# Optimization experiments

Measured on AMD Instinct MI355X. Metric: run time of the kernel, lower is better.

## Reference

```python
import jax, jax.numpy as jnp
import numpy as np

VOCAB, EMB, HID, LAYERS, SEQ, BATCH = 10000, 1024, 1024, 2, 64, 64


def setup_inputs() -> dict:
    key = jax.random.key(0)
    ks = jax.random.split(key, 12)
    b = 1.0 / np.sqrt(HID)
    u = lambda k, shape, bd: jax.random.uniform(k, shape, jnp.float32, -bd, bd)
    return {
        "inputs": jax.random.randint(ks[0], (SEQ, BATCH), 0, VOCAB),
        "hidden": jnp.zeros((LAYERS, BATCH, HID), jnp.float32),
        "emb": u(ks[1], (VOCAB, EMB), 0.1),
        "W0": u(ks[2], (EMB, 3 * HID), b),
        "U0": u(ks[3], (HID, 3 * HID), b),
        "bw0": u(ks[4], (3 * HID,), b),
        "bu0": u(ks[5], (3 * HID,), b),
        "W1": u(ks[6], (HID, 3 * HID), b),
        "U1": u(ks[7], (HID, 3 * HID), b),
        "bw1": u(ks[8], (3 * HID,), b),
        "bu1": u(ks[9], (3 * HID,), b),
        "fcW": u(ks[10], (VOCAB, HID), 0.1),
        "fcb": jnp.zeros((VOCAB,), jnp.float32),
    }


def gru_cell(x, h, W, U, bw, bu):
    gx = x @ W + bw            # [B, 3H]
    gh = h @ U + bu            # [B, 3H]
    i_r, i_z, i_n = jnp.split(gx, 3, axis=1)
    h_r, h_z, h_n = jnp.split(gh, 3, axis=1)
    r = jax.nn.sigmoid(i_r + h_r)
    z = jax.nn.sigmoid(i_z + h_z)
    h_tilde = jnp.tanh(i_n + r * h_n)
    return (1.0 - z) * h + z * h_tilde


def reference(inputs, hidden, emb, W0, U0, bw0, bu0, W1, U1, bw1, bu1, fcW, fcb):
    # dp_keep_prob = 1.0 -> dropout is identity (eval-mode reference)
    def step(hid, tok):
        x = emb[tok]                                   # [B, EMB]
        h0 = gru_cell(x, hid[0], W0, U0, bw0, bu0)     # [B, H]
        h1 = gru_cell(h0, hid[1], W1, U1, bw1, bu1)    # [B, H]
        y = h1 @ fcW.T + fcb                           # [B, V]
        return jnp.stack([h0, h1]), y

    hidden_f, logits = jax.lax.scan(step, hidden, inputs)
    return logits, hidden_f
```

## Files before the change

kernel.cpp:

```cpp
#include <hip/hip_runtime.h>
#include <math.h>

#define SEQL 64
#define BATCHN 64
#define HID 1024
#define EMBD 1024
#define VOCAB 10000
#define G3 3072
#define NPAD 10240
#define AROWS 4096
#define HSLOT 65536

typedef float f4v __attribute__((ext_vector_type(4)));
typedef unsigned short us4 __attribute__((ext_vector_type(4)));
typedef unsigned short us8 __attribute__((ext_vector_type(8)));
typedef __bf16 bf8v __attribute__((ext_vector_type(8)));

__device__ __forceinline__ unsigned short f2bf(float f) {
    unsigned u = __float_as_uint(f);
    u += 0x7fffu + ((u >> 16) & 1u);
    return (unsigned short)(u >> 16);
}
__device__ __forceinline__ float bf2f(unsigned short h) {
    return __uint_as_float(((unsigned)h) << 16);
}
__device__ __forceinline__ void split2(float f, unsigned short &hi, unsigned short &lo) {
    hi = f2bf(f);
    lo = f2bf(f - bf2f(hi));
}
__device__ __forceinline__ f4v mfma16(us8 a, us8 b, f4v c) {
    return __builtin_amdgcn_mfma_f32_16x16x32_bf16(
        __builtin_bit_cast(bf8v, a), __builtin_bit_cast(bf8v, b), c, 0, 0, 0);
}
__device__ __forceinline__ float sigmoidf_(float x) { return 1.f / (1.f + expf(-x)); }

__device__ __forceinline__ size_t htile_off(int b, int j) {
    return ((size_t)((((b >> 4) * 32 + (j >> 5)) * 64) + ((j >> 3) & 3) * 16 + (b & 15))) * 8 + (j & 7);
}

__global__ __launch_bounds__(256)
void tile_weights_kernel(const float* __restrict__ U0, const float* __restrict__ W1,
                         const float* __restrict__ U1, const float* __restrict__ W0,
                         unsigned short* __restrict__ hi, unsigned short* __restrict__ lo)
{
    __shared__ float tile[32][65];
    const int mat = blockIdx.z;
    const float* src = (mat == 0) ? U0 : (mat == 1) ? W1 : (mat == 2) ? U1 : W0;
    const int n0 = blockIdx.x * 64, k0 = blockIdx.y * 32;
    const int t = threadIdx.x, tx = t & 63, ty = t >> 6;
#pragma unroll
    for (int s = 0; s < 8; s++)
        tile[ty * 8 + s][tx] = src[(size_t)(k0 + ty * 8 + s) * G3 + n0 + tx];
    __syncthreads();
    const int c = t >> 6, lane = t & 63, fr = lane & 15, kg = lane >> 4;
    const int cc = (n0 >> 4) + c;
    const size_t off = (((size_t)(mat * 192 + cc) * 32 + (k0 >> 5)) * 64 + lane) * 8;
    us8 h8, l8;
#pragma unroll
    for (int e = 0; e < 8; e++) {
        unsigned short a, b;
        split2(tile[kg * 8 + e][c * 16 + fr], a, b);
        h8[e] = a; l8[e] = b;
    }
    *(us8*)(hi + off) = h8;
    *(us8*)(lo + off) = l8;
}

__global__ void fc_pad_split_kernel(const float* __restrict__ fcW,
                                    unsigned short* __restrict__ hi, unsigned short* __restrict__ lo)
{
    size_t i = ((size_t)blockIdx.x * 256 + threadIdx.x) * 4;
    size_t row = i >> 10;
    f4v v = {0.f, 0.f, 0.f, 0.f};
    if (row < VOCAB) v = *(const f4v*)(fcW + i);
    us4 h, l;
#pragma unroll
    for (int j = 0; j < 4; j++) { unsigned short a, b; split2(v[j], a, b); h[j] = a; l[j] = b; }
    *(us4*)(hi + i) = h;
    *(us4*)(lo + i) = l;
}

__global__ void fcb_pad_kernel(const float* __restrict__ fcb, float* __restrict__ fcb_pad)
{
    int idx = blockIdx.x * 256 + threadIdx.x;
    if (idx < NPAD) fcb_pad[idx] = (idx < VOCAB) ? fcb[idx] : 0.f;
}

__global__ void small_prep_kernel(const float* __restrict__ hidden,
                                  unsigned short* __restrict__ h0th, unsigned short* __restrict__ h0tl,
                                  unsigned short* __restrict__ h1th, unsigned short* __restrict__ h1tl)
{
    int idx = blockIdx.x * 256 + threadIdx.x;
    if (idx < BATCHN * HID) {
        int b = idx >> 10, j = idx & 1023;
        size_t o = htile_off(b, j);
        unsigned short a1, b1;
        split2(hidden[idx], a1, b1);                 h0th[o] = a1; h0tl[o] = b1;
        split2(hidden[BATCHN * HID + idx], a1, b1);  h1th[o] = a1; h1tl[o] = b1;
    }
}

__global__ __launch_bounds__(256)
void gx0_gemm_kernel(const int* __restrict__ tok, const float* __restrict__ emb,
                     const unsigned short* __restrict__ Wthi, const unsigned short* __restrict__ Wtlo,
                     float* __restrict__ C)
{
    __shared__ unsigned short Ah[128][40], Al[128][40];
    const int bswz = blockIdx.x;
    const int xcd = bswz & 7, s = bswz >> 3;
    const int col0 = (xcd + 8 * (s >> 5)) * 128;
    const int row0 = (s & 31) * 128;
    const int tid = threadIdx.x;
    const int lane = tid & 63, wave = tid >> 6;
    const int wm = wave >> 1, wn = wave & 1;
    const int srow = tid >> 1;
    const int shalf = (tid & 1) * 16;

    const float* asrc = emb + (size_t)tok[row0 + srow] * EMBD + shalf;
    const int fr = lane & 15, fk = (lane >> 4) * 8;
    const int cc0 = (col0 >> 4) + wn * 4;

    f4v a[4];
#pragma unroll
    for (int q = 0; q < 4; q++) a[q] = *(const f4v*)(asrc + q * 4);

    f4v acc[4][4] = {};
    for (int k0 = 0; k0 < EMBD; k0 += 32) {
        __syncthreads();
        us8 ahv[2], alv[2];
#pragma unroll
        for (int q = 0; q < 4; q++)
#pragma unroll
            for (int j = 0; j < 4; j++) {
                unsigned short h, l;
                split2(a[q][j], h, l);
                ahv[q >> 1][(q & 1) * 4 + j] = h;
                alv[q >> 1][(q & 1) * 4 + j] = l;
            }
        *(us8*)(&Ah[srow][shalf]) = ahv[0];     *(us8*)(&Ah[srow][shalf + 8]) = ahv[1];
        *(us8*)(&Al[srow][shalf]) = alv[0];     *(us8*)(&Al[srow][shalf + 8]) = alv[1];
        __syncthreads();
        if (k0 + 32 < EMBD) {
#pragma unroll
            for (int q = 0; q < 4; q++) a[q] = *(const f4v*)(asrc + k0 + 32 + q * 4);
        }
        const int ks = k0 >> 5;
        us8 bfh[4], bfl[4];
#pragma unroll
        for (int n = 0; n < 4; n++) {
            const size_t bo = (((size_t)(3 * 192 + cc0 + n) * 32 + ks) * 64 + lane) * 8;
            bfh[n] = *(const us8*)(Wthi + bo);
            bfl[n] = *(const us8*)(Wtlo + bo);
        }
        us8 afh[4], afl[4];
#pragma unroll
        for (int m = 0; m < 4; m++) {
            afh[m] = *(const us8*)(&Ah[wm * 64 + m * 16 + fr][fk]);
            afl[m] = *(const us8*)(&Al[wm * 64 + m * 16 + fr][fk]);
        }
#pragma unroll
        for (int n = 0; n < 4; n++)
#pragma unroll
            for (int m = 0; m < 4; m++) {
                acc[m][n] = mfma16(afh[m], bfh[n], acc[m][n]);
                acc[m][n] = mfma16(afh[m], bfl[n], acc[m][n]);
                acc[m][n] = mfma16(afl[m], bfh[n], acc[m][n]);
            }
    }
    const int fq = lane >> 4;
#pragma unroll
    for (int m = 0; m < 4; m++)
#pragma unroll
        for (int n = 0; n < 4; n++)
#pragma unroll
            for (int i = 0; i < 4; i++) {
                int r = row0 + wm * 64 + m * 16 + fq * 4 + i;
                int c = col0 + wn * 64 + n * 16 + fr;
                C[(size_t)r * G3 + c] = acc[m][n][i];
            }
}

__global__ __launch_bounds__(256)
void logits_gemm_kernel(const unsigned short* __restrict__ h1t_hi, const unsigned short* __restrict__ h1t_lo,
                        const unsigned short* __restrict__ Bhi, const unsigned short* __restrict__ Blo,
                        const float* __restrict__ bias, float* __restrict__ C)
{
    __shared__ unsigned short Bh[128][40], Bl[128][40];
    const int bswz = blockIdx.x;
    const int xcd = bswz & 7, s = bswz >> 3;
    const int col0 = (xcd + 8 * (s >> 5)) * 128;
    const int row0 = (s & 31) * 128;
    const int t0 = row0 >> 6;
    const int tid = threadIdx.x;
    const int lane = tid & 63, wave = tid >> 6;
    const int wm = wave >> 1, wn = wave & 1;
    const int srow = tid >> 1;
    const int shalf = (tid & 1) * 16;

    const unsigned short* bh_src = Bhi + (size_t)(col0 + srow) * HID + shalf;
    const unsigned short* bl_src = Blo + (size_t)(col0 + srow) * HID + shalf;

    f4v acc[4][4] = {};
    us8 bh2[2], bl2[2];
    bh2[0] = *(const us8*)(bh_src);  bh2[1] = *(const us8*)(bh_src + 8);
    bl2[0] = *(const us8*)(bl_src);  bl2[1] = *(const us8*)(bl_src + 8);

    const int fr = lane & 15, fk = (lane >> 4) * 8;
    const size_t abase = ((size_t)(t0 + wm) * 128) * 512 + (size_t)lane * 8;

    for (int k0 = 0; k0 < HID; k0 += 32) {
        __syncthreads();
        *(us8*)(&Bh[srow][shalf]) = bh2[0];  *(us8*)(&Bh[srow][shalf + 8]) = bh2[1];
        *(us8*)(&Bl[srow][shalf]) = bl2[0];  *(us8*)(&Bl[srow][shalf + 8]) = bl2[1];
        __syncthreads();
        if (k0 + 32 < HID) {
            bh2[0] = *(const us8*)(bh_src + k0 + 32);  bh2[1] = *(const us8*)(bh_src + k0 + 40);
            bl2[0] = *(const us8*)(bl_src + k0 + 32);  bl2[1] = *(const us8*)(bl_src + k0 + 40);
        }
        const int ks = k0 >> 5;
        us8 afh[4], afl[4];
#pragma unroll
        for (int m = 0; m < 4; m++) {
            const size_t ao = abase + (size_t)(m * 32 + ks) * 512;
            afh[m] = *(const us8*)(h1t_hi + ao);
            afl[m] = *(const us8*)(h1t_lo + ao);
        }
#pragma unroll
        for (int n = 0; n < 4; n++) {
            us8 bfh = *(const us8*)(&Bh[wn * 64 + n * 16 + fr][fk]);
            us8 bfl = *(const us8*)(&Bl[wn * 64 + n * 16 + fr][fk]);
#pragma unroll
            for (int m = 0; m < 4; m++) {
                acc[m][n] = mfma16(afh[m], bfh, acc[m][n]);
                acc[m][n] = mfma16(afh[m], bfl, acc[m][n]);
                acc[m][n] = mfma16(afl[m], bfh, acc[m][n]);
            }
        }
    }
    const int fq = lane >> 4;
#pragma unroll
    for (int m = 0; m < 4; m++)
#pragma unroll
        for (int n = 0; n < 4; n++)
#pragma unroll
            for (int i = 0; i < 4; i++) {
                int r = row0 + wm * 64 + m * 16 + fq * 4 + i;
                int c = col0 + wn * 64 + n * 16 + fr;
                float v = acc[m][n][i] + bias[c];
                if (c < VOCAB) C[(size_t)r * VOCAB + c] = v;
            }
}

template <bool DO_L0, bool DO_L1>
__global__ __launch_bounds__(512)
void step_kernel(const unsigned short* __restrict__ h0hi, const unsigned short* __restrict__ h0lo,
                 const unsigned short* __restrict__ h1hi, const unsigned short* __restrict__ h1lo,
                 const unsigned short* __restrict__ Wthi, const unsigned short* __restrict__ Wtlo,
                 const float* __restrict__ gx0next,
                 const float* __restrict__ bw0, const float* __restrict__ bu0,
                 const float* __restrict__ bw1, const float* __restrict__ bu1,
                 unsigned short* __restrict__ h0o_hi, unsigned short* __restrict__ h0o_lo,
                 unsigned short* __restrict__ h1o_hi, unsigned short* __restrict__ h1o_lo)
{
    __shared__ float red[4][9][16][17];
    const int tid = threadIdx.x, lane = tid & 63, wave = tid >> 6;
    const int bswz = blockIdx.x;
    const int xcd = bswz & 7, sb = bswz >> 3;
    const int jc = xcd + 8 * (sb >> 2);
    const int wr = sb & 3;
    const int j0 = jc * 16;
    const int T0 = DO_L0 ? 0 : 3, T1 = DO_L1 ? 9 : 3;

    f4v acc[9] = {};
#pragma unroll 2
    for (int ksl = 0; ksl < 4; ksl++) {
        const int ks = wave * 4 + ksl;
        const size_t aoff = ((size_t)(wr * 32 + ks) * 64 + lane) * 8;
        us8 a0h = *(const us8*)(h0hi + aoff);
        us8 a0l = *(const us8*)(h0lo + aoff);
        us8 a1h = {}, a1l = {};
        if (DO_L1) { a1h = *(const us8*)(h1hi + aoff); a1l = *(const us8*)(h1lo + aoff); }
#pragma unroll
        for (int g = 0; g < 3; g++) {
            const size_t base = (((size_t)(g * 64 + jc) * 32 + ks) * 64 + lane) * 8;
            if (DO_L0) {
                us8 bh = *(const us8*)(Wthi + base);
                us8 bl = *(const us8*)(Wtlo + base);
                acc[g] = mfma16(a0h, bh, acc[g]);
                acc[g] = mfma16(a0h, bl, acc[g]);
                acc[g] = mfma16(a0l, bh, acc[g]);
            }
            if (DO_L1) {
                const size_t b1 = base + (size_t)192 * 32 * 64 * 8;
                us8 bh = *(const us8*)(Wthi + b1);
                us8 bl = *(const us8*)(Wtlo + b1);
                acc[3 + g] = mfma16(a0h, bh, acc[3 + g]);
                acc[3 + g] = mfma16(a0h, bl, acc[3 + g]);
                acc[3 + g] = mfma16(a0l, bh, acc[3 + g]);
                const size_t b2 = base + (size_t)2 * 192 * 32 * 64 * 8;
                us8 ch = *(const us8*)(Wthi + b2);
                us8 cl = *(const us8*)(Wtlo + b2);
                acc[6 + g] = mfma16(a1h, ch, acc[6 + g]);
                acc[6 + g] = mfma16(a1h, cl, acc[6 + g]);
                acc[6 + g] = mfma16(a1l, ch, acc[6 + g]);
            }
        }
    }
    const int rrow = (lane >> 4) * 4, rcol = lane & 15;
    if (wave >= 4) {
#pragma unroll
        for (int t2 = 0; t2 < 9; t2++) if (t2 >= T0 && t2 < T1)
#pragma unroll
            for (int i = 0; i < 4; i++) red[wave - 4][t2][rrow + i][rcol] = acc[t2][i];
    }
    __syncthreads();
    if (wave < 4) {
#pragma unroll
        for (int t2 = 0; t2 < 9; t2++) if (t2 >= T0 && t2 < T1)
#pragma unroll
            for (int i = 0; i < 4; i++)
                red[wave][t2][rrow + i][rcol] += acc[t2][i];
    }
    __syncthreads();
    if (tid < 256) {
        const int bl_ = tid >> 4, jl = tid & 15;
        const int b = wr * 16 + bl_, j = j0 + jl;
        float G[9];
#pragma unroll
        for (int t2 = 0; t2 < 9; t2++) if (t2 >= T0 && t2 < T1)
            G[t2] = (red[0][t2][bl_][jl] + red[1][t2][bl_][jl])
                  + (red[2][t2][bl_][jl] + red[3][t2][bl_][jl]);
        const size_t po = htile_off(b, j);
        if (DO_L0) {
            float sr = gx0next[(size_t)b * G3 + j]            + bw0[j]           + G[0] + bu0[j];
            float sz = gx0next[(size_t)b * G3 + HID + j]      + bw0[HID + j]     + G[1] + bu0[HID + j];
            float gxn = gx0next[(size_t)b * G3 + 2 * HID + j] + bw0[2 * HID + j];
            float ghn = G[2] + bu0[2 * HID + j];
            float r = sigmoidf_(sr);
            float z = sigmoidf_(sz);
            float ht = tanhf(gxn + r * ghn);
            float hp = bf2f(h0hi[po]) + bf2f(h0lo[po]);
            float hn = (1.f - z) * hp + z * ht;
            unsigned short hh, hl2; split2(hn, hh, hl2);
            h0o_hi[po] = hh; h0o_lo[po] = hl2;
        }
        if (DO_L1) {
            float sr = G[3] + bw1[j]           + G[6] + bu1[j];
            float sz = G[4] + bw1[HID + j]     + G[7] + bu1[HID + j];
            float gxn = G[5] + bw1[2 * HID + j];
            float ghn = G[8] + bu1[2 * HID + j];
            float r = sigmoidf_(sr);
            float z = sigmoidf_(sz);
            float ht = tanhf(gxn + r * ghn);
            float hp = bf2f(h1hi[po]) + bf2f(h1lo[po]);
            float hn = (1.f - z) * hp + z * ht;
            unsigned short hh, hl2; split2(hn, hh, hl2);
            h1o_hi[po] = hh; h1o_lo[po] = hl2;
        }
    }
}

__global__ void hidden_out_kernel(const unsigned short* __restrict__ h0hi, const unsigned short* __restrict__ h0lo,
                                  const unsigned short* __restrict__ h1hi, const unsigned short* __restrict__ h1lo,
                                  float* __restrict__ out)
{
    int i = blockIdx.x * 256 + threadIdx.x;
    if (i < BATCHN * HID) {
        int b = i >> 10, j = i & 1023;
        size_t o = htile_off(b, j);
        out[i] = bf2f(h0hi[o]) + bf2f(h0lo[o]);
        out[BATCHN * HID + i] = bf2f(h1hi[o]) + bf2f(h1lo[o]);
    }
}

extern "C" void kernel_launch(void* const* d_in, const int* in_sizes, int n_in,
                              void* d_out, int out_size, void* d_ws, size_t ws_size,
                              hipStream_t stream)
{
    (void)in_sizes; (void)n_in; (void)out_size;
    const int*   tok    = (const int*)  d_in[0];
    const float* hidden = (const float*)d_in[1];
    const float* emb    = (const float*)d_in[2];
    const float* W0     = (const float*)d_in[3];
    const float* U0     = (const float*)d_in[4];
    const float* bw0    = (const float*)d_in[5];
    const float* bu0    = (const float*)d_in[6];
    const float* W1     = (const float*)d_in[7];
    const float* U1     = (const float*)d_in[8];
    const float* bw1    = (const float*)d_in[9];
    const float* bu1    = (const float*)d_in[10];
    const float* fcW    = (const float*)d_in[11];
    const float* fcb    = (const float*)d_in[12];
    float* out = (float*)d_out;

    char* wsp = (char*)d_ws;
    size_t used = 0;
    auto alloc = [&](size_t bytes) -> char* {
        char* p = wsp + used;
        used += (bytes + 255) & ~(size_t)255;
        return p;
    };
    unsigned short* Wt_hi = (unsigned short*)alloc((size_t)4 * G3 * HID * 2);
    unsigned short* Wt_lo = (unsigned short*)alloc((size_t)4 * G3 * HID * 2);
    float*          GX0   = (float*)alloc((size_t)AROWS * G3 * 4);
    unsigned short* H0Thi = (unsigned short*)alloc((size_t)SEQL * HSLOT * 2);
    unsigned short* H0Tlo = (unsigned short*)alloc((size_t)SEQL * HSLOT * 2);
    unsigned short* H1Thi = (unsigned short*)alloc((size_t)SEQL * HSLOT * 2);
    unsigned short* H1Tlo = (unsigned short*)alloc((size_t)SEQL * HSLOT * 2);
    unsigned short* h0ith = (unsigned short*)alloc((size_t)HSLOT * 2);
    unsigned short* h0itl = (unsigned short*)alloc((size_t)HSLOT * 2);
    unsigned short* h1ith = (unsigned short*)alloc((size_t)HSLOT * 2);
    unsigned short* h1itl = (unsigned short*)alloc((size_t)HSLOT * 2);
    if (used > ws_size) return;

    unsigned short* fcWhi = Wt_hi;
    unsigned short* fcWlo = Wt_lo;
    float*          fcbp  = (float*)((char*)Wt_hi + (size_t)NPAD * HID * 2);

    tile_weights_kernel<<<dim3(48, 32, 4), 256, 0, stream>>>(U0, W1, U1, W0, Wt_hi, Wt_lo);
    small_prep_kernel<<<256, 256, 0, stream>>>(hidden, h0ith, h0itl, h1ith, h1itl);
    gx0_gemm_kernel<<<768, 256, 0, stream>>>(tok, emb, Wt_hi, Wt_lo, GX0);

    step_kernel<true, false><<<256, 512, 0, stream>>>(
        h0ith, h0itl, h1ith, h1itl, Wt_hi, Wt_lo,
        GX0, bw0, bu0, bw1, bu1,
        H0Thi, H0Tlo,
        H1Thi + (size_t)63 * HSLOT, H1Tlo + (size_t)63 * HSLOT);

    for (int t = 0; t < 63; t++) {
        const unsigned short* a1h = (t == 0) ? h1ith : H1Thi + (size_t)(t - 1) * HSLOT;
        const unsigned short* a1l = (t == 0) ? h1itl : H1Tlo + (size_t)(t - 1) * HSLOT;
        step_kernel<true, true><<<256, 512, 0, stream>>>(
            H0Thi + (size_t)t * HSLOT, H0Tlo + (size_t)t * HSLOT,
            a1h, a1l,
            Wt_hi, Wt_lo,
            GX0 + (size_t)(t + 1) * BATCHN * G3, bw0, bu0, bw1, bu1,
            H0Thi + (size_t)(t + 1) * HSLOT, H0Tlo + (size_t)(t + 1) * HSLOT,
            H1Thi + (size_t)t * HSLOT, H1Tlo + (size_t)t * HSLOT);
    }
    step_kernel<false, true><<<256, 512, 0, stream>>>(
        H0Thi + (size_t)63 * HSLOT, H0Tlo + (size_t)63 * HSLOT,
        H1Thi + (size_t)62 * HSLOT, H1Tlo + (size_t)62 * HSLOT,
        Wt_hi, Wt_lo,
        GX0, bw0, bu0, bw1, bu1,
        h0ith, h0itl,
        H1Thi + (size_t)63 * HSLOT, H1Tlo + (size_t)63 * HSLOT);

    hidden_out_kernel<<<256, 256, 0, stream>>>(
        H0Thi + (size_t)63 * HSLOT, H0Tlo + (size_t)63 * HSLOT,
        H1Thi + (size_t)63 * HSLOT, H1Tlo + (size_t)63 * HSLOT,
        out + (size_t)AROWS * VOCAB);

    fc_pad_split_kernel<<<NPAD, 256, 0, stream>>>(fcW, fcWhi, fcWlo);
    fcb_pad_kernel<<<(NPAD + 255) / 256, 256, 0, stream>>>(fcb, fcbp);
    logits_gemm_kernel<<<2560, 256, 0, stream>>>(
        H1Thi, H1Tlo, fcWhi, fcWlo, fcbp, out);
}
```

Before: 1.836 ms.

## Split recurrent step into split-K GEMM kernel plus separate reduce/gate kernel

Each timestep's fused GEMM+gate kernel becomes two launches. The first uses a 4-way split-K across blocks, with each block covering all 64 batch rows for one 16-column chunk, and writes partial sums to a global buffer. The second kernel reduces the four partials and applies the GRU gates. This reuses the weight tile across all batch rows within a block instead of reloading it per batch quarter, at the cost of a second launch per step and extra global traffic for the partial sums.

Measured after the change: 1.695 ms. 1.08x faster.

```diff
diff --git a/kernel.cpp b/kernel.cpp
--- a/kernel.cpp
+++ b/kernel.cpp
@@ -251,46 +251,38 @@
             }
 }
 
-template <bool DO_L0, bool DO_L1>
+template <int T0, int T1>
 __global__ __launch_bounds__(512)
-void step_kernel(const unsigned short* __restrict__ h0hi, const unsigned short* __restrict__ h0lo,
-                 const unsigned short* __restrict__ h1hi, const unsigned short* __restrict__ h1lo,
-                 const unsigned short* __restrict__ Wthi, const unsigned short* __restrict__ Wtlo,
-                 const float* __restrict__ gx0next,
-                 const float* __restrict__ bw0, const float* __restrict__ bu0,
-                 const float* __restrict__ bw1, const float* __restrict__ bu1,
-                 unsigned short* __restrict__ h0o_hi, unsigned short* __restrict__ h0o_lo,
-                 unsigned short* __restrict__ h1o_hi, unsigned short* __restrict__ h1o_lo)
+void step_gemm_kernel(const unsigned short* __restrict__ h0hi, const unsigned short* __restrict__ h0lo,
+                      const unsigned short* __restrict__ h1hi, const unsigned short* __restrict__ h1lo,
+                      const unsigned short* __restrict__ Wthi, const unsigned short* __restrict__ Wtlo,
+                      float* __restrict__ P)
 {
     __shared__ float red[4][9][16][17];
     const int tid = threadIdx.x, lane = tid & 63, wave = tid >> 6;
-    const int bswz = blockIdx.x;
-    const int xcd = bswz & 7, sb = bswz >> 3;
-    const int jc = xcd + 8 * (sb >> 2);
-    const int wr = sb & 3;
-    const int j0 = jc * 16;
-    const int T0 = DO_L0 ? 0 : 3, T1 = DO_L1 ? 9 : 3;
+    const int wr = wave & 3, kh = wave >> 2;
+    const int jc = blockIdx.x >> 2, kq = blockIdx.x & 3;
 
     f4v acc[9] = {};
-#pragma unroll 2
+#pragma unroll
     for (int ksl = 0; ksl < 4; ksl++) {
-        const int ks = wave * 4 + ksl;
+        const int ks = kq * 8 + kh * 4 + ksl;
         const size_t aoff = ((size_t)(wr * 32 + ks) * 64 + lane) * 8;
         us8 a0h = *(const us8*)(h0hi + aoff);
         us8 a0l = *(const us8*)(h0lo + aoff);
         us8 a1h = {}, a1l = {};
-        if (DO_L1) { a1h = *(const us8*)(h1hi + aoff); a1l = *(const us8*)(h1lo + aoff); }
+        if (T1 > 3) { a1h = *(const us8*)(h1hi + aoff); a1l = *(const us8*)(h1lo + aoff); }
 #pragma unroll
         for (int g = 0; g < 3; g++) {
             const size_t base = (((size_t)(g * 64 + jc) * 32 + ks) * 64 + lane) * 8;
-            if (DO_L0) {
+            if (T0 == 0) {
                 us8 bh = *(const us8*)(Wthi + base);
                 us8 bl = *(const us8*)(Wtlo + base);
                 acc[g] = mfma16(a0h, bh, acc[g]);
                 acc[g] = mfma16(a0h, bl, acc[g]);
                 acc[g] = mfma16(a0l, bh, acc[g]);
             }
-            if (DO_L1) {
+            if (T1 > 3) {
                 const size_t b1 = base + (size_t)192 * 32 * 64 * 8;
                 us8 bh = *(const us8*)(Wthi + b1);
                 us8 bl = *(const us8*)(Wtlo + b1);
@@ -307,56 +299,70 @@
         }
     }
     const int rrow = (lane >> 4) * 4, rcol = lane & 15;
-    if (wave >= 4) {
-#pragma unroll
-        for (int t2 = 0; t2 < 9; t2++) if (t2 >= T0 && t2 < T1)
-#pragma unroll
-            for (int i = 0; i < 4; i++) red[wave - 4][t2][rrow + i][rcol] = acc[t2][i];
+    if (kh == 1) {
+#pragma unroll
+        for (int t2 = T0; t2 < T1; t2++)
+#pragma unroll
+            for (int i = 0; i < 4; i++) red[wr][t2][rrow + i][rcol] = acc[t2][i];
     }
     __syncthreads();
-    if (wave < 4) {
-#pragma unroll
-        for (int t2 = 0; t2 < 9; t2++) if (t2 >= T0 && t2 < T1)
-#pragma unroll
-            for (int i = 0; i < 4; i++)
-                red[wave][t2][rrow + i][rcol] += acc[t2][i];
-    }
-    __syncthreads();
-    if (tid < 256) {
-        const int bl_ = tid >> 4, jl = tid & 15;
-        const int b = wr * 16 + bl_, j = j0 + jl;
-        float G[9];
-#pragma unroll
-        for (int t2 = 0; t2 < 9; t2++) if (t2 >= T0 && t2 < T1)
-            G[t2] = (red[0][t2][bl_][jl] + red[1][t2][bl_][jl])
-                  + (red[2][t2][bl_][jl] + red[3][t2][bl_][jl]);
-        const size_t po = htile_off(b, j);
-        if (DO_L0) {
-            float sr = gx0next[(size_t)b * G3 + j]            + bw0[j]           + G[0] + bu0[j];
-            float sz = gx0next[(size_t)b * G3 + HID + j]      + bw0[HID + j]     + G[1] + bu0[HID + j];
-            float gxn = gx0next[(size_t)b * G3 + 2 * HID + j] + bw0[2 * HID + j];
-            float ghn = G[2] + bu0[2 * HID + j];
-            float r = sigmoidf_(sr);
-            float z = sigmoidf_(sz);
-            float ht = tanhf(gxn + r * ghn);
-            float hp = bf2f(h0hi[po]) + bf2f(h0lo[po]);
-            float hn = (1.f - z) * hp + z * ht;
-            unsigned short hh, hl2; split2(hn, hh, hl2);
-            h0o_hi[po] = hh; h0o_lo[po] = hl2;
-        }
-        if (DO_L1) {
-            float sr = G[3] + bw1[j]           + G[6] + bu1[j];
-            float sz = G[4] + bw1[HID + j]     + G[7] + bu1[HID + j];
-            float gxn = G[5] + bw1[2 * HID + j];
-            float ghn = G[8] + bu1[2 * HID + j];
-            float r = sigmoidf_(sr);
-            float z = sigmoidf_(sz);
-            float ht = tanhf(gxn + r * ghn);
-            float hp = bf2f(h1hi[po]) + bf2f(h1lo[po]);
-            float hn = (1.f - z) * hp + z * ht;
-            unsigned short hh, hl2; split2(hn, hh, hl2);
-            h1o_hi[po] = hh; h1o_lo[po] = hl2;
-        }
+    if (kh == 0) {
+#pragma unroll
+        for (int t2 = T0; t2 < T1; t2++)
+#pragma unroll
+            for (int i = 0; i < 4; i++) {
+                float v = acc[t2][i] + red[wr][t2][rrow + i][rcol];
+                const int b = wr * 16 + rrow + i;
+                P[(((size_t)kq * 9 + t2) * 64 + b) * 1024 + jc * 16 + rcol] = v;
+            }
+    }
+}
+
+template <int T0, int T1>
+__global__ __launch_bounds__(256)
+void step_reduce_kernel(const float* __restrict__ P, const float* __restrict__ gx0next,
+                        const float* __restrict__ bw0, const float* __restrict__ bu0,
+                        const float* __restrict__ bw1, const float* __restrict__ bu1,
+                        const unsigned short* __restrict__ h0hi, const unsigned short* __restrict__ h0lo,
+                        const unsigned short* __restrict__ h1hi, const unsigned short* __restrict__ h1lo,
+                        unsigned short* __restrict__ h0o_hi, unsigned short* __restrict__ h0o_lo,
+                        unsigned short* __restrict__ h1o_hi, unsigned short* __restrict__ h1o_lo)
+{
+    const int idx = blockIdx.x * 256 + threadIdx.x;
+    const int b = idx >> 10, j = idx & 1023;
+    float G[9];
+#pragma unroll
+    for (int t2 = T0; t2 < T1; t2++) {
+        const float* p = P + ((size_t)t2 * 64 + b) * 1024 + j;
+        G[t2] = (p[0] + p[(size_t)9 * 64 * 1024])
+              + (p[(size_t)18 * 64 * 1024] + p[(size_t)27 * 64 * 1024]);
+    }
+    const size_t po = htile_off(b, j);
+    if (T0 == 0) {
+        float sr  = gx0next[(size_t)b * G3 + j]            + bw0[j]           + G[0] + bu0[j];
+        float sz  = gx0next[(size_t)b * G3 + HID + j]      + bw0[HID + j]     + G[1] + bu0[HID + j];
+        float gxn = gx0next[(size_t)b * G3 + 2 * HID + j]  + bw0[2 * HID + j];
+        float ghn = G[2] + bu0[2 * HID + j];
+        float r = sigmoidf_(sr);
+        float z = sigmoidf_(sz);
+        float ht = tanhf(gxn + r * ghn);
+        float hp = bf2f(h0hi[po]) + bf2f(h0lo[po]);
+        float hn = (1.f - z) * hp + z * ht;
+        unsigned short hh, hl2; split2(hn, hh, hl2);
+        h0o_hi[po] = hh; h0o_lo[po] = hl2;
+    }
+    if (T1 > 3) {
+        float sr  = G[3] + bw1[j]           + G[6] + bu1[j];
+        float sz  = G[4] + bw1[HID + j]     + G[7] + bu1[HID + j];
+        float gxn = G[5] + bw1[2 * HID + j];
+        float ghn = G[8] + bu1[2 * HID + j];
+        float r = sigmoidf_(sr);
+        float z = sigmoidf_(sz);
+        float ht = tanhf(gxn + r * ghn);
+        float hp = bf2f(h1hi[po]) + bf2f(h1lo[po]);
+        float hn = (1.f - z) * hp + z * ht;
+        unsigned short hh, hl2; split2(hn, hh, hl2);
+        h1o_hi[po] = hh; h1o_lo[po] = hl2;
     }
 }
 
@@ -407,6 +413,8 @@
     unsigned short* H0Tlo = (unsigned short*)alloc((size_t)SEQL * HSLOT * 2);
     unsigned short* H1Thi = (unsigned short*)alloc((size_t)SEQL * HSLOT * 2);
     unsigned short* H1Tlo = (unsigned short*)alloc((size_t)SEQL * HSLOT * 2);
+    float*          P0    = (float*)alloc((size_t)4 * 9 * BATCHN * HID * 4);
+    float*          P1    = (float*)alloc((size_t)4 * 9 * BATCHN * HID * 4);
     unsigned short* h0ith = (unsigned short*)alloc((size_t)HSLOT * 2);
     unsigned short* h0itl = (unsigned short*)alloc((size_t)HSLOT * 2);
     unsigned short* h1ith = (unsigned short*)alloc((size_t)HSLOT * 2);
@@ -421,28 +429,36 @@
     small_prep_kernel<<<256, 256, 0, stream>>>(hidden, h0ith, h0itl, h1ith, h1itl);
     gx0_gemm_kernel<<<768, 256, 0, stream>>>(tok, emb, Wt_hi, Wt_lo, GX0);
 
-    step_kernel<true, false><<<256, 512, 0, stream>>>(
-        h0ith, h0itl, h1ith, h1itl, Wt_hi, Wt_lo,
-        GX0, bw0, bu0, bw1, bu1,
+    step_gemm_kernel<0, 3><<<256, 512, 0, stream>>>(
+        h0ith, h0itl, h1ith, h1itl, Wt_hi, Wt_lo, P0);
+    step_reduce_kernel<0, 3><<<256, 256, 0, stream>>>(
+        P0, GX0, bw0, bu0, bw1, bu1,
+        h0ith, h0itl, h1ith, h1itl,
         H0Thi, H0Tlo,
         H1Thi + (size_t)63 * HSLOT, H1Tlo + (size_t)63 * HSLOT);
 
     for (int t = 0; t < 63; t++) {
+        const unsigned short* h0h = H0Thi + (size_t)t * HSLOT;
+        const unsigned short* h0l = H0Tlo + (size_t)t * HSLOT;
         const unsigned short* a1h = (t == 0) ? h1ith : H1Thi + (size_t)(t - 1) * HSLOT;
         const unsigned short* a1l = (t == 0) ? h1itl : H1Tlo + (size_t)(t - 1) * HSLOT;
-        step_kernel<true, true><<<256, 512, 0, stream>>>(
-            H0Thi + (size_t)t * HSLOT, H0Tlo + (size_t)t * HSLOT,
-            a1h, a1l,
-            Wt_hi, Wt_lo,
-            GX0 + (size_t)(t + 1) * BATCHN * G3, bw0, bu0, bw1, bu1,
+        float* Pb = ((t & 1) == 0) ? P1 : P0;
+        step_gemm_kernel<0, 9><<<256, 512, 0, stream>>>(
+            h0h, h0l, a1h, a1l, Wt_hi, Wt_lo, Pb);
+        step_reduce_kernel<0, 9><<<256, 256, 0, stream>>>(
+            Pb, GX0 + (size_t)(t + 1) * BATCHN * G3, bw0, bu0, bw1, bu1,
+            h0h, h0l, a1h, a1l,
             H0Thi + (size_t)(t + 1) * HSLOT, H0Tlo + (size_t)(t + 1) * HSLOT,
             H1Thi + (size_t)t * HSLOT, H1Tlo + (size_t)t * HSLOT);
     }
-    step_kernel<false, true><<<256, 512, 0, stream>>>(
+    step_gemm_kernel<3, 9><<<256, 512, 0, stream>>>(
         H0Thi + (size_t)63 * HSLOT, H0Tlo + (size_t)63 * HSLOT,
         H1Thi + (size_t)62 * HSLOT, H1Tlo + (size_t)62 * HSLOT,
-        Wt_hi, Wt_lo,
-        GX0, bw0, bu0, bw1, bu1,
+        Wt_hi, Wt_lo, P0);
+    step_reduce_kernel<3, 9><<<256, 256, 0, stream>>>(
+        P0, GX0, bw0, bu0, bw1, bu1,
+        H0Thi + (size_t)63 * HSLOT, H0Tlo + (size_t)63 * HSLOT,
+        H1Thi + (size_t)62 * HSLOT, H1Tlo + (size_t)62 * HSLOT,
         h0ith, h0itl,
         H1Thi + (size_t)63 * HSLOT, H1Tlo + (size_t)63 * HSLOT);
 
```
